# Performance work log

Measured on AMD Instinct MI355X. Metric: run time of the kernel, lower is better.

## Reference

```python
import jax, jax.numpy as jnp
import numpy as np

N = 50000       # num_entities / nodes
E = 100000      # edges
K = 8           # incoming edge-graph neighbors per edge
D_NODE = 64
D_EDGE = 64
H = 4
DH = D_EDGE // H
DIN = D_EDGE + 2 * D_NODE  # [edge_feat, node_feat[src], node_feat[dst]]


def setup_inputs() -> dict:
    key = jax.random.key(0)
    ks = jax.random.split(key, 6)
    node_features = jax.random.normal(ks[0], (N, D_NODE), jnp.float32)
    edge_features = jax.random.normal(ks[1], (E, D_EDGE), jnp.float32)
    edge_index = jax.random.randint(ks[2], (2, E), 0, N)
    node_tiers = jax.random.randint(ks[3], (N,), 0, 4, dtype=jnp.int32)
    # edge adjacency (line graph): each edge attends to K other edges
    adj_dst = jnp.repeat(jnp.arange(E), K)                       # [A]
    adj_src = jax.random.randint(ks[4], (E * K,), 0, E)          # [A]
    # learned params: two EdgeAttention layers, each Wq/Wk/Wv [DIN,D_EDGE], Wo [D_EDGE,D_EDGE]
    wkeys = jax.random.split(ks[5], 8)
    def w(k, fan_in, fan_out):
        return jax.random.normal(k, (fan_in, fan_out), jnp.float32) * np.float32(1.0 / np.sqrt(fan_in))
    params = {}
    for li in (1, 2):
        base = (li - 1) * 4
        params[f'l{li}_Wq'] = w(wkeys[base + 0], DIN, D_EDGE)
        params[f'l{li}_Wk'] = w(wkeys[base + 1], DIN, D_EDGE)
        params[f'l{li}_Wv'] = w(wkeys[base + 2], DIN, D_EDGE)
        params[f'l{li}_Wo'] = w(wkeys[base + 3], D_EDGE, D_EDGE)
    return dict(node_features=node_features, edge_features=edge_features,
                edge_index=edge_index, node_tiers=node_tiers,
                adj_src=adj_src, adj_dst=adj_dst, **params)


def _edge_attention(node_f, edge_f, edge_index, adj_src, adj_dst, Wq, Wk, Wv, Wo):
    # x: edge feature conditioned on endpoint node features  [E, DIN]
    x = jnp.concatenate([edge_f, node_f[edge_index[0]], node_f[edge_index[1]]], axis=-1)
    q = (x @ Wq).reshape(E, H, DH)
    k = (x @ Wk).reshape(E, H, DH)
    v = (x @ Wv).reshape(E, H, DH)
    scale = np.float32(1.0 / np.sqrt(DH))
    # scores per adjacency pair  [A, H]
    s = jnp.einsum('ahd,ahd->ah', q[adj_dst], k[adj_src]) * scale
    # segment softmax over incoming neighbors of each dst edge
    m = jax.ops.segment_max(s, adj_dst, num_segments=E)          # [E, H]
    e = jnp.exp(s - m[adj_dst])                                   # [A, H]
    denom = jax.ops.segment_sum(e, adj_dst, num_segments=E)      # [E, H]
    alpha = e / denom[adj_dst]                                    # [A, H]
    out = jax.ops.segment_sum(alpha[..., None] * v[adj_src], adj_dst, num_segments=E)  # [E,H,DH]
    return edge_f + out.reshape(E, D_EDGE) @ Wo                   # residual


def reference(node_features, edge_features, edge_index, node_tiers, adj_src, adj_dst,
              l1_Wq, l1_Wk, l1_Wv, l1_Wo, l2_Wq, l2_Wk, l2_Wv, l2_Wo):
    ef = _edge_attention(node_features, edge_features, edge_index, adj_src, adj_dst,
                         l1_Wq, l1_Wk, l1_Wv, l1_Wo)
    ef = _edge_attention(node_features, ef, edge_index, adj_src, adj_dst,
                         l2_Wq, l2_Wk, l2_Wv, l2_Wo)
    return ef  # updated edge features of the output DeltaGraph
```

## Files before the change

kernel.cpp:

```cpp
#include <hip/hip_runtime.h>

#define NE 100000
#define NN 50000
#define NT 1563
#define GRID_QKV 512

typedef short short8 __attribute__((ext_vector_type(8)));
typedef float f32x4 __attribute__((ext_vector_type(4)));
typedef unsigned short ushort;
typedef unsigned int uint;

__device__ inline ushort f2bf(float f) {
    unsigned int u = __float_as_uint(f);
    u += 0x7FFFu + ((u >> 16) & 1u);
    return (ushort)(u >> 16);
}
__device__ inline float bf2f(ushort u) {
    return __uint_as_float((unsigned int)u << 16);
}

__device__ inline short8 pack_bf8(float4 a, float4 b) {
    short8 r;
    r[0] = (short)f2bf(a.x); r[1] = (short)f2bf(a.y);
    r[2] = (short)f2bf(a.z); r[3] = (short)f2bf(a.w);
    r[4] = (short)f2bf(b.x); r[5] = (short)f2bf(b.y);
    r[6] = (short)f2bf(b.z); r[7] = (short)f2bf(b.w);
    return r;
}

__device__ inline void pack_qkv_slot(int slot, const float* Wq, const float* Wk,
                                     const float* Wv, ushort* wf)
{
    int lane = slot & 63;
    int st = slot >> 6;
    int s = st / 12, t = st % 12;
    int n = t * 16 + (lane & 15);
    int kb = s * 32 + (lane >> 4) * 8;
    const float* w = (n < 64) ? Wq : (n < 128) ? Wk : Wv;
    int nn = n & 63;
    #pragma unroll
    for (int j = 0; j < 8; ++j)
        wf[(size_t)slot * 8 + j] = f2bf(w[(size_t)(kb + j) * 64 + nn]);
}

__device__ inline void pack_wo_slot(int slot, const float* Wo, ushort* wf)
{
    int lane = slot & 63;
    int st = slot >> 6;
    int s = st / 4, t = st % 4;
    int n = t * 16 + (lane & 15);
    int kb = s * 32 + (lane >> 4) * 8;
    #pragma unroll
    for (int j = 0; j < 8; ++j)
        wf[(size_t)slot * 8 + j] = f2bf(Wo[(size_t)(kb + j) * 64 + n]);
}

__global__ __launch_bounds__(256) void prep_all(
    const float* __restrict__ l1Wq, const float* __restrict__ l1Wk,
    const float* __restrict__ l1Wv, const float* __restrict__ l1Wo,
    const float* __restrict__ l2Wq, const float* __restrict__ l2Wk,
    const float* __restrict__ l2Wv, const float* __restrict__ l2Wo,
    ushort* __restrict__ wf1, ushort* __restrict__ wf2,
    ushort* __restrict__ wo1, ushort* __restrict__ wo2)
{
    int idx = blockIdx.x * 256 + threadIdx.x;
    if (idx < 4608)            pack_qkv_slot(idx,         l1Wq, l1Wk, l1Wv, wf1);
    else if (idx < 9216)       pack_qkv_slot(idx - 4608,  l2Wq, l2Wk, l2Wv, wf2);
    else if (idx < 9728)       pack_wo_slot (idx - 9216,  l1Wo, wo1);
    else if (idx < 10240)      pack_wo_slot (idx - 9728,  l2Wo, wo2);
}

#define MFMA_B16(a, b, c) c = __builtin_amdgcn_mfma_f32_16x16x32_bf16(a, b, c, 0, 0, 0)
#define GLP const __attribute__((address_space(1))) uint*
#define LDP __attribute__((address_space(3))) uint*

__global__ __launch_bounds__(256) void qkv_mfma(
    const float* __restrict__ ef, const float* __restrict__ nodef,
    const int* __restrict__ eidx, const ushort* __restrict__ wfrag,
    ushort* __restrict__ qo, ushort* __restrict__ ko, ushort* __restrict__ vo)
{
    __shared__ __align__(1024) char ldsb[72 * 1024];

    const int tid = threadIdx.x;
    const int l   = tid & 63;
    const int w   = tid >> 6;
    const int r   = l & 15;
    const int kg  = l >> 4;
    const int koff = kg * 8;

    #pragma unroll 1
    for (int i = 0; i < 18; ++i) {
        const int fr = w * 18 + i;
        __builtin_amdgcn_global_load_lds(
            (GLP)((const char*)wfrag + (size_t)fr * 1024 + (size_t)l * 16),
            (LDP)(ldsb + (size_t)fr * 1024 + (size_t)l * 16), 16, 0, 0);
    }
    __syncthreads();

    #pragma unroll 1
    for (int tile = blockIdx.x; tile < NT; tile += GRID_QKV) {
        const int e0 = tile * 64 + w * 16;
        const int e  = e0 + r;
        const int ec = (e < NE) ? e : NE - 1;
        const float* rp0 = ef    + (size_t)ec * 64;
        const float* rp1 = nodef + (size_t)eidx[ec] * 64;
        const float* rp2 = nodef + (size_t)eidx[NE + ec] * 64;

        f32x4 acc[12];
        #pragma unroll
        for (int t = 0; t < 12; ++t) acc[t] = (f32x4)(0.f);

        #pragma unroll 1
        for (int s = 0; s < 6; ++s) {
            const float* bp = ((s < 2) ? rp0 : (s < 4) ? rp1 : rp2)
                              + (s & 1) * 32 + koff;
            short8 A = pack_bf8(*(const float4*)bp, *(const float4*)(bp + 4));
            const char* lb = ldsb + (size_t)s * 12288 + (size_t)l * 16;
            #pragma unroll
            for (int t = 0; t < 12; ++t) {
                short8 b = *(const short8*)(lb + (size_t)t * 1024);
                MFMA_B16(A, b, acc[t]);
            }
        }

        const int orow = e0 + kg * 4;
        #pragma unroll
        for (int t = 0; t < 12; ++t) {
            ushort* dst = (t < 4) ? qo : (t < 8) ? ko : vo;
            ushort* dp  = dst + (t & 3) * 16 + r;
            #pragma unroll
            for (int j = 0; j < 4; ++j) {
                const int row = orow + j;
                if (row < NE) dp[(size_t)row * 64] = f2bf(acc[t][j]);
            }
        }
    }
}

__global__ __launch_bounds__(256) void attn_kernel(
    const ushort* __restrict__ q, const ushort* __restrict__ kbuf,
    const ushort* __restrict__ vbuf, const int* __restrict__ adj_src,
    ushort* __restrict__ ao)
{
    const int wid  = (blockIdx.x * 256 + threadIdx.x) >> 6;
    const int lane = threadIdx.x & 63;
    if (wid >= NE) return;
    const int e    = wid;
    const int half = lane >> 5;
    const int l32  = lane & 31;

    const int4 nb = *(const int4*)(adj_src + e * 8 + half * 4);
    const int nbr0 = nb.x, nbr1 = nb.y, nbr2 = nb.z, nbr3 = nb.w;

    ushort2 qu = *(const ushort2*)(q + (size_t)e * 64 + l32 * 2);
    const float q0 = bf2f(qu.x), q1 = bf2f(qu.y);

    ushort2 ku0 = *(const ushort2*)(kbuf + (size_t)nbr0 * 64 + l32 * 2);
    ushort2 ku1 = *(const ushort2*)(kbuf + (size_t)nbr1 * 64 + l32 * 2);
    ushort2 ku2 = *(const ushort2*)(kbuf + (size_t)nbr2 * 64 + l32 * 2);
    ushort2 ku3 = *(const ushort2*)(kbuf + (size_t)nbr3 * 64 + l32 * 2);
    ushort2 vu0 = *(const ushort2*)(vbuf + (size_t)nbr0 * 64 + l32 * 2);
    ushort2 vu1 = *(const ushort2*)(vbuf + (size_t)nbr1 * 64 + l32 * 2);
    ushort2 vu2 = *(const ushort2*)(vbuf + (size_t)nbr2 * 64 + l32 * 2);
    ushort2 vu3 = *(const ushort2*)(vbuf + (size_t)nbr3 * 64 + l32 * 2);

    float s0 = q0 * bf2f(ku0.x) + q1 * bf2f(ku0.y);
    float s1 = q0 * bf2f(ku1.x) + q1 * bf2f(ku1.y);
    float s2 = q0 * bf2f(ku2.x) + q1 * bf2f(ku2.y);
    float s3 = q0 * bf2f(ku3.x) + q1 * bf2f(ku3.y);
    s0 += __shfl_xor(s0, 1); s0 += __shfl_xor(s0, 2); s0 += __shfl_xor(s0, 4);
    s1 += __shfl_xor(s1, 1); s1 += __shfl_xor(s1, 2); s1 += __shfl_xor(s1, 4);
    s2 += __shfl_xor(s2, 1); s2 += __shfl_xor(s2, 2); s2 += __shfl_xor(s2, 4);
    s3 += __shfl_xor(s3, 1); s3 += __shfl_xor(s3, 2); s3 += __shfl_xor(s3, 4);
    s0 *= 0.25f; s1 *= 0.25f; s2 *= 0.25f; s3 *= 0.25f;

    float m = fmaxf(fmaxf(s0, s1), fmaxf(s2, s3));
    m = fmaxf(m, __shfl_xor(m, 32));
    float w0 = __expf(s0 - m), w1 = __expf(s1 - m);
    float w2 = __expf(s2 - m), w3 = __expf(s3 - m);
    float den = w0 + w1 + w2 + w3;
    den += __shfl_xor(den, 32);
    const float inv = 1.f / den;

    float ox = 0.f, oy = 0.f;
    ox = fmaf(w0, bf2f(vu0.x), ox); oy = fmaf(w0, bf2f(vu0.y), oy);
    ox = fmaf(w1, bf2f(vu1.x), ox); oy = fmaf(w1, bf2f(vu1.y), oy);
    ox = fmaf(w2, bf2f(vu2.x), ox); oy = fmaf(w2, bf2f(vu2.y), oy);
    ox = fmaf(w3, bf2f(vu3.x), ox); oy = fmaf(w3, bf2f(vu3.y), oy);
    ox = (ox + __shfl_xor(ox, 32)) * inv;
    oy = (oy + __shfl_xor(oy, 32)) * inv;

    if (lane < 32) {
        ushort2 o;
        o.x = f2bf(ox);
        o.y = f2bf(oy);
        *(ushort2*)(ao + (size_t)e * 64 + l32 * 2) = o;
    }
}

__global__ __launch_bounds__(256) void wo_mfma(
    const float* __restrict__ ef_in, const ushort* __restrict__ attn,
    const ushort* __restrict__ wofrag, float* __restrict__ efo)
{
    const int wave = threadIdx.x >> 6;
    const int lane = threadIdx.x & 63;
    const int r  = lane & 15;
    const int kg = lane >> 4;
    const int e0 = blockIdx.x * 64 + wave * 16;
    const int e  = e0 + r;
    const int ec = (e < NE) ? e : NE - 1;

    short8 af0 = *(const short8*)(attn + (size_t)ec * 64 + kg * 8);
    short8 af1 = *(const short8*)(attn + (size_t)ec * 64 + 32 + kg * 8);

    const char* wf = (const char*)wofrag + (size_t)lane * 16;
    f32x4 d0 = (f32x4)(0.f), d1 = (f32x4)(0.f), d2 = (f32x4)(0.f), d3 = (f32x4)(0.f);
    short8 g0 = *(const short8*)(wf + 0 * 1024);
    short8 g1 = *(const short8*)(wf + 1 * 1024);
    short8 g2 = *(const short8*)(wf + 2 * 1024);
    short8 g3 = *(const short8*)(wf + 3 * 1024);
    MFMA_B16(af0, g0, d0); MFMA_B16(af0, g1, d1);
    MFMA_B16(af0, g2, d2); MFMA_B16(af0, g3, d3);
    g0 = *(const short8*)(wf + 4 * 1024);
    g1 = *(const short8*)(wf + 5 * 1024);
    g2 = *(const short8*)(wf + 6 * 1024);
    g3 = *(const short8*)(wf + 7 * 1024);
    MFMA_B16(af1, g0, d0); MFMA_B16(af1, g1, d1);
    MFMA_B16(af1, g2, d2); MFMA_B16(af1, g3, d3);

    const int orow = e0 + kg * 4;
    #pragma unroll
    for (int t = 0; t < 4; ++t) {
        const f32x4 dd = (t == 0) ? d0 : (t == 1) ? d1 : (t == 2) ? d2 : d3;
        const int c = t * 16 + r;
        #pragma unroll
        for (int j = 0; j < 4; ++j) {
            int row = orow + j;
            if (row < NE) {
                size_t off = (size_t)row * 64 + c;
                efo[off] = dd[j] + ef_in[off];
            }
        }
    }
}

extern "C" void kernel_launch(void* const* d_in, const int* in_sizes, int n_in,
                              void* d_out, int out_size, void* d_ws, size_t ws_size,
                              hipStream_t stream)
{
    const float* nodef   = (const float*)d_in[0];
    const float* ef      = (const float*)d_in[1];
    const int*   eidx    = (const int*)d_in[2];
    const int*   adj_src = (const int*)d_in[4];
    const float* l1Wq = (const float*)d_in[6];
    const float* l1Wk = (const float*)d_in[7];
    const float* l1Wv = (const float*)d_in[8];
    const float* l1Wo = (const float*)d_in[9];
    const float* l2Wq = (const float*)d_in[10];
    const float* l2Wk = (const float*)d_in[11];
    const float* l2Wv = (const float*)d_in[12];
    const float* l2Wo = (const float*)d_in[13];

    ushort* q   = (ushort*)d_ws;
    ushort* k   = q   + (size_t)NE * 64;
    ushort* v   = k   + (size_t)NE * 64;
    ushort* ao  = v   + (size_t)NE * 64;
    ushort* wf1 = ao  + (size_t)NE * 64;
    ushort* wf2 = wf1 + 36864;
    ushort* wo1 = wf2 + 36864;
    ushort* wo2 = wo1 + 4096;
    float* out = (float*)d_out;

    dim3 blk(256);
    const int ga = (NE + 3) / 4;
    const int gw = (NE + 63) / 64;

    prep_all<<<40, blk, 0, stream>>>(l1Wq, l1Wk, l1Wv, l1Wo,
                                     l2Wq, l2Wk, l2Wv, l2Wo,
                                     wf1, wf2, wo1, wo2);

    qkv_mfma<<<GRID_QKV, blk, 0, stream>>>(ef, nodef, eidx, wf1, q, k, v);
    attn_kernel<<<ga, blk, 0, stream>>>(q, k, v, adj_src, ao);
    wo_mfma<<<gw, blk, 0, stream>>>(ef, ao, wo1, out);
    qkv_mfma<<<GRID_QKV, blk, 0, stream>>>(out, nodef, eidx, wf2, q, k, v);
    attn_kernel<<<ga, blk, 0, stream>>>(q, k, v, adj_src, ao);
    wo_mfma<<<gw, blk, 0, stream>>>(out, ao, wo2, out);
}
```

Baseline: 153.1 us.

## Split QKV projection by output columns across waves, drop LDS weight staging

The persistent QKV kernel, which staged all weight fragments into 72KB of LDS, is replaced by one-shot kernels. Each wave computes 3 of the 12 output column tiles for 16 (or 32) rows and reads weight fragments directly from global/L2. This removes the per-block LDS fill and the low occupancy caused by the large shared-memory footprint, and it adds many more blocks. In exchange, each row's gathered inputs are loaded redundantly by all four waves and weights are re-read per block from cache. The first layer uses a 16-row variant and the second a 32-row variant.

```diff
diff --git a/kernel.cpp b/kernel.cpp
--- a/kernel.cpp
+++ b/kernel.cpp
@@ -2,8 +2,6 @@
 
 #define NE 100000
 #define NN 50000
-#define NT 1563
-#define GRID_QKV 512
 
 typedef short short8 __attribute__((ext_vector_type(8)));
 typedef float f32x4 __attribute__((ext_vector_type(4)));
@@ -71,67 +69,130 @@
 }
 
 #define MFMA_B16(a, b, c) c = __builtin_amdgcn_mfma_f32_16x16x32_bf16(a, b, c, 0, 0, 0)
-#define GLP const __attribute__((address_space(1))) uint*
-#define LDP __attribute__((address_space(3))) uint*
-
-__global__ __launch_bounds__(256) void qkv_mfma(
+
+#define QS16(s, Areg) do {                                                     \
+    short8 b0 = *(const short8*)(wfb + (size_t)(s) * 12288);                   \
+    short8 b1 = *(const short8*)(wfb + (size_t)(s) * 12288 + 1024);            \
+    short8 b2 = *(const short8*)(wfb + (size_t)(s) * 12288 + 2048);            \
+    MFMA_B16(Areg, b0, c0); MFMA_B16(Areg, b1, c1); MFMA_B16(Areg, b2, c2);    \
+} while (0)
+
+__global__ __launch_bounds__(256) void qkv16(
     const float* __restrict__ ef, const float* __restrict__ nodef,
     const int* __restrict__ eidx, const ushort* __restrict__ wfrag,
     ushort* __restrict__ qo, ushort* __restrict__ ko, ushort* __restrict__ vo)
 {
-    __shared__ __align__(1024) char ldsb[72 * 1024];
-
     const int tid = threadIdx.x;
     const int l   = tid & 63;
     const int w   = tid >> 6;
     const int r   = l & 15;
     const int kg  = l >> 4;
+    const int e0  = blockIdx.x * 16;
+    const int e   = e0 + r;
+    const int ec  = (e < NE) ? e : NE - 1;
     const int koff = kg * 8;
 
-    #pragma unroll 1
-    for (int i = 0; i < 18; ++i) {
-        const int fr = w * 18 + i;
-        __builtin_amdgcn_global_load_lds(
-            (GLP)((const char*)wfrag + (size_t)fr * 1024 + (size_t)l * 16),
-            (LDP)(ldsb + (size_t)fr * 1024 + (size_t)l * 16), 16, 0, 0);
+    const float* rp0 = ef    + (size_t)ec * 64;
+    const float* rp1 = nodef + (size_t)eidx[ec] * 64;
+    const float* rp2 = nodef + (size_t)eidx[NE + ec] * 64;
+
+    short8 A0 = pack_bf8(*(const float4*)(rp0 + koff),      *(const float4*)(rp0 + koff + 4));
+    short8 A1 = pack_bf8(*(const float4*)(rp0 + 32 + koff), *(const float4*)(rp0 + 36 + koff));
+    short8 A2 = pack_bf8(*(const float4*)(rp1 + koff),      *(const float4*)(rp1 + koff + 4));
+    short8 A3 = pack_bf8(*(const float4*)(rp1 + 32 + koff), *(const float4*)(rp1 + 36 + koff));
+    short8 A4 = pack_bf8(*(const float4*)(rp2 + koff),      *(const float4*)(rp2 + koff + 4));
+    short8 A5 = pack_bf8(*(const float4*)(rp2 + 32 + koff), *(const float4*)(rp2 + 36 + koff));
+
+    f32x4 c0 = (f32x4)(0.f), c1 = (f32x4)(0.f), c2 = (f32x4)(0.f);
+    const char* wfb = (const char*)wfrag + (size_t)(3 * w) * 1024 + (size_t)l * 16;
+
+    QS16(0, A0); QS16(1, A1); QS16(2, A2);
+    QS16(3, A3); QS16(4, A4); QS16(5, A5);
+
+    const int orow = e0 + kg * 4;
+    #pragma unroll
+    for (int n = 0; n < 3; ++n) {
+        const int T = 3 * w + n;
+        const f32x4 cc = (n == 0) ? c0 : (n == 1) ? c1 : c2;
+        ushort* dst = (T < 4) ? (qo + T * 16) : (T < 8) ? (ko + (T - 4) * 16)
+                                              : (vo + (T - 8) * 16);
+        ushort* dp = dst + r;
+        #pragma unroll
+        for (int j = 0; j < 4; ++j) {
+            const int row = orow + j;
+            if (row < NE) dp[(size_t)row * 64] = f2bf(cc[j]);
+        }
     }
-    __syncthreads();
-
-    #pragma unroll 1
-    for (int tile = blockIdx.x; tile < NT; tile += GRID_QKV) {
-        const int e0 = tile * 64 + w * 16;
-        const int e  = e0 + r;
-        const int ec = (e < NE) ? e : NE - 1;
-        const float* rp0 = ef    + (size_t)ec * 64;
-        const float* rp1 = nodef + (size_t)eidx[ec] * 64;
-        const float* rp2 = nodef + (size_t)eidx[NE + ec] * 64;
-
-        f32x4 acc[12];
+}
+
+#define QS32(s, Aa, Ab) do {                                                   \
+    short8 b0 = *(const short8*)(wfb + (size_t)(s) * 12288);                   \
+    short8 b1 = *(const short8*)(wfb + (size_t)(s) * 12288 + 1024);            \
+    short8 b2 = *(const short8*)(wfb + (size_t)(s) * 12288 + 2048);            \
+    MFMA_B16(Aa, b0, c00); MFMA_B16(Aa, b1, c01); MFMA_B16(Aa, b2, c02);       \
+    MFMA_B16(Ab, b0, c10); MFMA_B16(Ab, b1, c11); MFMA_B16(Ab, b2, c12);       \
+} while (0)
+
+__global__ __launch_bounds__(256) void qkv32(
+    const float* __restrict__ ef, const float* __restrict__ nodef,
+    const int* __restrict__ eidx, const ushort* __restrict__ wfrag,
+    ushort* __restrict__ qo, ushort* __restrict__ ko, ushort* __restrict__ vo)
+{
+    const int tid = threadIdx.x;
+    const int l   = tid & 63;
+    const int w   = tid >> 6;
+    const int r   = l & 15;
+    const int kg  = l >> 4;
+    const int e0  = blockIdx.x * 32;
+    const int ea  = e0 + r;
+    const int eb  = e0 + 16 + r;
+    const int eac = (ea < NE) ? ea : NE - 1;
+    const int ebc = (eb < NE) ? eb : NE - 1;
+    const int koff = kg * 8;
+
+    const float* pa0 = ef    + (size_t)eac * 64;
+    const float* pa1 = nodef + (size_t)eidx[eac] * 64;
+    const float* pa2 = nodef + (size_t)eidx[NE + eac] * 64;
+    const float* pb0 = ef    + (size_t)ebc * 64;
+    const float* pb1 = nodef + (size_t)eidx[ebc] * 64;
+    const float* pb2 = nodef + (size_t)eidx[NE + ebc] * 64;
+
+    short8 Aa0 = pack_bf8(*(const float4*)(pa0 + koff),      *(const float4*)(pa0 + koff + 4));
+    short8 Aa1 = pack_bf8(*(const float4*)(pa0 + 32 + koff), *(const float4*)(pa0 + 36 + koff));
+    short8 Aa2 = pack_bf8(*(const float4*)(pa1 + koff),      *(const float4*)(pa1 + koff + 4));
+    short8 Aa3 = pack_bf8(*(const float4*)(pa1 + 32 + koff), *(const float4*)(pa1 + 36 + koff));
+    short8 Aa4 = pack_bf8(*(const float4*)(pa2 + koff),      *(const float4*)(pa2 + koff + 4));
+    short8 Aa5 = pack_bf8(*(const float4*)(pa2 + 32 + koff), *(const float4*)(pa2 + 36 + koff));
+    short8 Ab0 = pack_bf8(*(const float4*)(pb0 + koff),      *(const float4*)(pb0 + koff + 4));
+    short8 Ab1 = pack_bf8(*(const float4*)(pb0 + 32 + koff), *(const float4*)(pb0 + 36 + koff));
+    short8 Ab2 = pack_bf8(*(const float4*)(pb1 + koff),      *(const float4*)(pb1 + koff + 4));
+    short8 Ab3 = pack_bf8(*(const float4*)(pb1 + 32 + koff), *(const float4*)(pb1 + 36 + koff));
+    short8 Ab4 = pack_bf8(*(const float4*)(pb2 + koff),      *(const float4*)(pb2 + koff + 4));
+    short8 Ab5 = pack_bf8(*(const float4*)(pb2 + 32 + koff), *(const float4*)(pb2 + 36 + koff));
+
+    f32x4 c00 = (f32x4)(0.f), c01 = (f32x4)(0.f), c02 = (f32x4)(0.f);
+    f32x4 c10 = (f32x4)(0.f), c11 = (f32x4)(0.f), c12 = (f32x4)(0.f);
+    const char* wfb = (const char*)wfrag + (size_t)(3 * w) * 1024 + (size_t)l * 16;
+
+    QS32(0, Aa0, Ab0); QS32(1, Aa1, Ab1); QS32(2, Aa2, Ab2);
+    QS32(3, Aa3, Ab3); QS32(4, Aa4, Ab4); QS32(5, Aa5, Ab5);
+
+    #pragma unroll
+    for (int half = 0; half < 2; ++half) {
+        const int orow = e0 + half * 16 + kg * 4;
         #pragma unroll
-        for (int t = 0; t < 12; ++t) acc[t] = (f32x4)(0.f);
-
-        #pragma unroll 1
-        for (int s = 0; s < 6; ++s) {
-            const float* bp = ((s < 2) ? rp0 : (s < 4) ? rp1 : rp2)
-                              + (s & 1) * 32 + koff;
-            short8 A = pack_bf8(*(const float4*)bp, *(const float4*)(bp + 4));
-            const char* lb = ldsb + (size_t)s * 12288 + (size_t)l * 16;
-            #pragma unroll
-            for (int t = 0; t < 12; ++t) {
-                short8 b = *(const short8*)(lb + (size_t)t * 1024);
-                MFMA_B16(A, b, acc[t]);
-            }
-        }
-
-        const int orow = e0 + kg * 4;
-        #pragma unroll
-        for (int t = 0; t < 12; ++t) {
-            ushort* dst = (t < 4) ? qo : (t < 8) ? ko : vo;
-            ushort* dp  = dst + (t & 3) * 16 + r;
+        for (int n = 0; n < 3; ++n) {
+            const int T = 3 * w + n;
+            const f32x4 cc = (half == 0)
+                ? ((n == 0) ? c00 : (n == 1) ? c01 : c02)
+                : ((n == 0) ? c10 : (n == 1) ? c11 : c12);
+            ushort* dst = (T < 4) ? (qo + T * 16) : (T < 8) ? (ko + (T - 4) * 16)
+                                                  : (vo + (T - 8) * 16);
+            ushort* dp = dst + r;
             #pragma unroll
             for (int j = 0; j < 4; ++j) {
                 const int row = orow + j;
-                if (row < NE) dp[(size_t)row * 64] = f2bf(acc[t][j]);
+                if (row < NE) dp[(size_t)row * 64] = f2bf(cc[j]);
             }
         }
     }
@@ -272,17 +333,19 @@
     float* out = (float*)d_out;
 
     dim3 blk(256);
-    const int ga = (NE + 3) / 4;
-    const int gw = (NE + 63) / 64;
+    const int g16 = (NE + 15) / 16;
+    const int g32 = (NE + 31) / 32;
+    const int ga  = (NE + 3) / 4;
+    const int gw  = (NE + 63) / 64;
 
     prep_all<<<40, blk, 0, stream>>>(l1Wq, l1Wk, l1Wv, l1Wo,
                                      l2Wq, l2Wk, l2Wv, l2Wo,
                                      wf1, wf2, wo1, wo2);
 
-    qkv_mfma<<<GRID_QKV, blk, 0, stream>>>(ef, nodef, eidx, wf1, q, k, v);
+    qkv16<<<g16, blk, 0, stream>>>(ef, nodef, eidx, wf1, q, k, v);
     attn_kernel<<<ga, blk, 0, stream>>>(q, k, v, adj_src, ao);
     wo_mfma<<<gw, blk, 0, stream>>>(ef, ao, wo1, out);
-    qkv_mfma<<<GRID_QKV, blk, 0, stream>>>(out, nodef, eidx, wf2, q, k, v);
+    qkv32<<<g32, blk, 0, stream>>>(out, nodef, eidx, wf2, q, k, v);
     attn_kernel<<<ga, blk, 0, stream>>>(q, k, v, adj_src, ao);
     wo_mfma<<<gw, blk, 0, stream>>>(out, ao, wo2, out);
 }
```

Result: slower. 195.2 us (+27.4%).

## Software-pipeline QKV gather loads with register double-buffering across tiles

Applied to the files above, without the earlier changes.

Restructures the QKV MFMA kernel so the next tile's gathered edge and node feature rows are loaded into a second register set while the current tile is computed. It fully unrolls the six k-steps and the output stores, and sets launch_bounds occupancy to 2 blocks per CU. The aim is to hide global gather latency behind MFMA work. The cost is higher register pressure from 24 float4 prefetch registers plus 12 accumulators, which could cause spills or reduce occupancy. The 72KB of LDS per block may also cap occupancy regardless.

```diff
diff --git a/kernel.cpp b/kernel.cpp
--- a/kernel.cpp
+++ b/kernel.cpp
@@ -74,8 +74,66 @@
 #define GLP const __attribute__((address_space(1))) uint*
 #define LDP __attribute__((address_space(3))) uint*
 
-__global__ __launch_bounds__(256) void qkv_mfma(
-    const float* __restrict__ ef, const float* __restrict__ nodef,
+#define PRE(S, tl) do {                                                        \
+    const int e_  = (tl) * 64 + w * 16 + r;                                    \
+    const int ec_ = (e_ < NE) ? e_ : NE - 1;                                   \
+    const int sa_ = eidx[ec_];                                                 \
+    const int da_ = eidx[NE + ec_];                                            \
+    const float* p0_ = efin  + (size_t)ec_ * 64 + koff;                        \
+    const float* p1_ = nodef + (size_t)sa_ * 64 + koff;                        \
+    const float* p2_ = nodef + (size_t)da_ * 64 + koff;                        \
+    f##S##_0  = *(const float4*)(p0_);      f##S##_1  = *(const float4*)(p0_ + 4);  \
+    f##S##_2  = *(const float4*)(p0_ + 32); f##S##_3  = *(const float4*)(p0_ + 36); \
+    f##S##_4  = *(const float4*)(p1_);      f##S##_5  = *(const float4*)(p1_ + 4);  \
+    f##S##_6  = *(const float4*)(p1_ + 32); f##S##_7  = *(const float4*)(p1_ + 36); \
+    f##S##_8  = *(const float4*)(p2_);      f##S##_9  = *(const float4*)(p2_ + 4);  \
+    f##S##_10 = *(const float4*)(p2_ + 32); f##S##_11 = *(const float4*)(p2_ + 36); \
+} while (0)
+
+#define K12(s, Areg) do {                                                      \
+    const char* lb_ = ldsb + (size_t)(s) * 12288 + (size_t)l * 16;             \
+    MFMA_B16(Areg, *(const short8*)(lb_ +     0), c0);                         \
+    MFMA_B16(Areg, *(const short8*)(lb_ +  1024), c1);                         \
+    MFMA_B16(Areg, *(const short8*)(lb_ +  2048), c2);                         \
+    MFMA_B16(Areg, *(const short8*)(lb_ +  3072), c3);                         \
+    MFMA_B16(Areg, *(const short8*)(lb_ +  4096), c4);                         \
+    MFMA_B16(Areg, *(const short8*)(lb_ +  5120), c5);                         \
+    MFMA_B16(Areg, *(const short8*)(lb_ +  6144), c6);                         \
+    MFMA_B16(Areg, *(const short8*)(lb_ +  7168), c7);                         \
+    MFMA_B16(Areg, *(const short8*)(lb_ +  8192), c8);                         \
+    MFMA_B16(Areg, *(const short8*)(lb_ +  9216), c9);                         \
+    MFMA_B16(Areg, *(const short8*)(lb_ + 10240), c10);                        \
+    MFMA_B16(Areg, *(const short8*)(lb_ + 11264), c11);                        \
+} while (0)
+
+#define STT(creg, dstp, coloff) do {                                           \
+    ushort* dp_ = (dstp) + (coloff) + r;                                       \
+    if (orow_ + 0 < NE) dp_[(size_t)(orow_ + 0) * 64] = f2bf(creg[0]);         \
+    if (orow_ + 1 < NE) dp_[(size_t)(orow_ + 1) * 64] = f2bf(creg[1]);         \
+    if (orow_ + 2 < NE) dp_[(size_t)(orow_ + 2) * 64] = f2bf(creg[2]);         \
+    if (orow_ + 3 < NE) dp_[(size_t)(orow_ + 3) * 64] = f2bf(creg[3]);         \
+} while (0)
+
+#define COMP(S, tl) do {                                                       \
+    f32x4 c0 = (f32x4)(0.f), c1 = (f32x4)(0.f), c2  = (f32x4)(0.f);            \
+    f32x4 c3 = (f32x4)(0.f), c4 = (f32x4)(0.f), c5  = (f32x4)(0.f);            \
+    f32x4 c6 = (f32x4)(0.f), c7 = (f32x4)(0.f), c8  = (f32x4)(0.f);            \
+    f32x4 c9 = (f32x4)(0.f), c10 = (f32x4)(0.f), c11 = (f32x4)(0.f);           \
+    short8 A_;                                                                 \
+    A_ = pack_bf8(f##S##_0,  f##S##_1);  K12(0, A_);                           \
+    A_ = pack_bf8(f##S##_2,  f##S##_3);  K12(1, A_);                           \
+    A_ = pack_bf8(f##S##_4,  f##S##_5);  K12(2, A_);                           \
+    A_ = pack_bf8(f##S##_6,  f##S##_7);  K12(3, A_);                           \
+    A_ = pack_bf8(f##S##_8,  f##S##_9);  K12(4, A_);                           \
+    A_ = pack_bf8(f##S##_10, f##S##_11); K12(5, A_);                           \
+    const int orow_ = (tl) * 64 + w * 16 + kg * 4;                             \
+    STT(c0,  qo,  0); STT(c1,  qo, 16); STT(c2,  qo, 32); STT(c3,  qo, 48);    \
+    STT(c4,  ko,  0); STT(c5,  ko, 16); STT(c6,  ko, 32); STT(c7,  ko, 48);    \
+    STT(c8,  vo,  0); STT(c9,  vo, 16); STT(c10, vo, 32); STT(c11, vo, 48);    \
+} while (0)
+
+__global__ __launch_bounds__(256, 2) void qkv_mfma(
+    const float* __restrict__ efin, const float* __restrict__ nodef,
     const int* __restrict__ eidx, const ushort* __restrict__ wfrag,
     ushort* __restrict__ qo, ushort* __restrict__ ko, ushort* __restrict__ vo)
 {
@@ -87,6 +145,7 @@
     const int r   = l & 15;
     const int kg  = l >> 4;
     const int koff = kg * 8;
+    const int bid = blockIdx.x;
 
     #pragma unroll 1
     for (int i = 0; i < 18; ++i) {
@@ -95,44 +154,31 @@
             (GLP)((const char*)wfrag + (size_t)fr * 1024 + (size_t)l * 16),
             (LDP)(ldsb + (size_t)fr * 1024 + (size_t)l * 16), 16, 0, 0);
     }
+
+    float4 fA_0, fA_1, fA_2, fA_3, fA_4, fA_5, fA_6, fA_7, fA_8, fA_9, fA_10, fA_11;
+    float4 fB_0, fB_1, fB_2, fB_3, fB_4, fB_5, fB_6, fB_7, fB_8, fB_9, fB_10, fB_11;
+
+    PRE(A, bid);
     __syncthreads();
 
     #pragma unroll 1
-    for (int tile = blockIdx.x; tile < NT; tile += GRID_QKV) {
-        const int e0 = tile * 64 + w * 16;
-        const int e  = e0 + r;
-        const int ec = (e < NE) ? e : NE - 1;
-        const float* rp0 = ef    + (size_t)ec * 64;
-        const float* rp1 = nodef + (size_t)eidx[ec] * 64;
-        const float* rp2 = nodef + (size_t)eidx[NE + ec] * 64;
-
-        f32x4 acc[12];
-        #pragma unroll
-        for (int t = 0; t < 12; ++t) acc[t] = (f32x4)(0.f);
-
-        #pragma unroll 1
-        for (int s = 0; s < 6; ++s) {
-            const float* bp = ((s < 2) ? rp0 : (s < 4) ? rp1 : rp2)
-                              + (s & 1) * 32 + koff;
-            short8 A = pack_bf8(*(const float4*)bp, *(const float4*)(bp + 4));
-            const char* lb = ldsb + (size_t)s * 12288 + (size_t)l * 16;
-            #pragma unroll
-            for (int t = 0; t < 12; ++t) {
-                short8 b = *(const short8*)(lb + (size_t)t * 1024);
-                MFMA_B16(A, b, acc[t]);
+    for (int i = 0; ; i += 2) {
+        const int tA = bid + i * GRID_QKV;
+        const int tB = tA + GRID_QKV;
+        if (tB < NT) {
+            PRE(B, tB);
+            COMP(A, tA);
+            const int tC = tB + GRID_QKV;
+            if (tC < NT) {
+                PRE(A, tC);
+                COMP(B, tB);
+            } else {
+                COMP(B, tB);
+                break;
             }
-        }
-
-        const int orow = e0 + kg * 4;
-        #pragma unroll
-        for (int t = 0; t < 12; ++t) {
-            ushort* dst = (t < 4) ? qo : (t < 8) ? ko : vo;
-            ushort* dp  = dst + (t & 3) * 16 + r;
-            #pragma unroll
-            for (int j = 0; j < 4; ++j) {
-                const int row = orow + j;
-                if (row < NE) dp[(size_t)row * 64] = f2bf(acc[t][j]);
-            }
+        } else {
+            COMP(A, tA);
+            break;
         }
     }
 }
```

After: 300.9 us. +96.5%, slower.
